# Performance work log

Hardware: AMD Instinct MI355X
Metric: run time of the kernel (lower is better)

Reference implementation:

```python
import jax, jax.numpy as jnp
import numpy as np

K = 10
ALPHA = 0.1
N_NODES = 100000
N_EDGES = 3200000
FEATURES = 512
HIDDEN = 256
CLASSES = 64


def setup_inputs() -> dict:
    key = jax.random.key(0)
    k1, k2, k3, k4 = jax.random.split(key, 4)
    x = jax.random.normal(k1, (N_NODES, FEATURES), dtype=jnp.float32)
    edge_index = jax.random.randint(k2, (2, N_EDGES), 0, N_NODES, dtype=jnp.int64)
    W1 = jax.random.normal(k3, (FEATURES, HIDDEN), dtype=jnp.float32) * (1.0 / np.sqrt(FEATURES))
    b1 = jnp.zeros((HIDDEN,), dtype=jnp.float32)
    W2 = jax.random.normal(k4, (HIDDEN, CLASSES), dtype=jnp.float32) * (1.0 / np.sqrt(HIDDEN))
    b2 = jnp.zeros((CLASSES,), dtype=jnp.float32)
    return {"x": x, "edge_index": edge_index, "W1": W1, "b1": b1, "W2": W2, "b2": b2}


def _gcn_norm(edge_index, n_nodes):
    # Add self-loops (APPNP / GCN normalization: D^-1/2 (A+I) D^-1/2)
    loops = jnp.arange(n_nodes, dtype=edge_index.dtype)
    row = jnp.concatenate([edge_index[0], loops])
    col = jnp.concatenate([edge_index[1], loops])
    ones = jnp.ones(row.shape[0], dtype=jnp.float32)
    deg = jax.ops.segment_sum(ones, col, num_segments=n_nodes)
    dinv = jnp.where(deg > 0, jax.lax.rsqrt(deg), 0.0)
    norm = dinv[row] * dinv[col]
    return row, col, norm


def reference(x, edge_index, W1, b1, W2, b2):
    n = x.shape[0]
    h = jax.nn.relu(x @ W1 + b1)          # [N, hidden]
    h = h @ W2 + b2                        # [N, classes]
    row, col, norm = _gcn_norm(edge_index, n)

    def step(out, _):
        msg = out[col] * norm[:, None]     # gather + scale over edges
        agg = jax.ops.segment_sum(msg, row, num_segments=n)
        return (1.0 - ALPHA) * agg + ALPHA * h, None

    out, _ = jax.lax.scan(step, h, None, length=K)
    return jax.nn.log_softmax(out, axis=1)
```

## Files before the change

### kernel.cpp

```cpp
#include <hip/hip_runtime.h>
#include <hip/hip_bf16.h>
#include <math.h>

#define N_NODES 100000
#define N_EDGES 3200000
#define FEAT 512
#define HID 256
#define CLS 64
#define K_ITER 10
#define NBUCK 196
#define BSH 9
#define CH 16384
#define NCHUNK 196

typedef _Float16 half8 __attribute__((ext_vector_type(8)));
typedef float f32x4 __attribute__((ext_vector_type(4)));

__device__ __forceinline__ int edge_at(const void* e, int is64, long long idx) {
    return is64 ? (int)((const long long*)e)[idx] : ((const int*)e)[idx];
}

__global__ void k_detect(const unsigned* __restrict__ e, int* __restrict__ flag,
                         int* __restrict__ bcntR, int* __restrict__ bcntC) {
    __shared__ unsigned s[256];
    unsigned v = 0;
    for (int i = threadIdx.x; i < 4096; i += 256) v |= e[2 * i + 1];
    s[threadIdx.x] = v;
    __syncthreads();
    for (int off = 128; off; off >>= 1) {
        if (threadIdx.x < off) s[threadIdx.x] |= s[threadIdx.x + off];
        __syncthreads();
    }
    if (threadIdx.x == 0) flag[0] = (s[0] == 0) ? 1 : 0;
    if (threadIdx.x < NBUCK) { bcntR[threadIdx.x] = 0; bcntC[threadIdx.x] = 0; }
}

__global__ __launch_bounds__(256) void k_bhist(const void* __restrict__ e,
                                               const int* __restrict__ flag,
                                               int* __restrict__ bcntR,
                                               int* __restrict__ bcntC,
                                               int* __restrict__ histR,
                                               int* __restrict__ histC) {
    __shared__ int lhR[NBUCK], lhC[NBUCK];
    for (int i = threadIdx.x; i < NBUCK; i += 256) { lhR[i] = 0; lhC[i] = 0; }
    __syncthreads();
    int is64 = flag[0];
    const int ch = blockIdx.x;
    long long base = (long long)ch * CH;
    for (int j = threadIdx.x; j < CH; j += 256) {
        long long i = base + j;
        if (i < N_EDGES) {
            int r = edge_at(e, is64, i);
            int c = edge_at(e, is64, (long long)N_EDGES + i);
            atomicAdd(&lhR[r >> BSH], 1);
            atomicAdd(&lhC[c >> BSH], 1);
        }
    }
    __syncthreads();
    for (int i = threadIdx.x; i < NBUCK; i += 256) {
        histR[ch * NBUCK + i] = lhR[i];
        histC[ch * NBUCK + i] = lhC[i];
        if (lhR[i]) atomicAdd(&bcntR[i], lhR[i]);
        if (lhC[i]) atomicAdd(&bcntC[i], lhC[i]);
    }
}

__global__ void k_bscan(const int* __restrict__ bcntR, const int* __restrict__ bcntC,
                        int* __restrict__ bbaseR, int* __restrict__ bbaseC,
                        int* __restrict__ cbase, int* __restrict__ offs) {
    if (threadIdx.x == 0) {
        int accE = 0, accC = 0, accCv = 0;
        for (int b = 0; b < NBUCK; b++) {
            bbaseR[b] = accE;
            bbaseC[b] = accCv;
            cbase[b] = accC;
            int nb0 = b << BSH;
            int nn = (N_NODES - nb0 < 512) ? (N_NODES - nb0) : 512;
            accE += bcntR[b];
            accCv += bcntC[b];
            accC += bcntR[b] + nn;
        }
        bbaseR[NBUCK] = accE;
        bbaseC[NBUCK] = accCv;
        cbase[NBUCK] = accC;
        offs[N_NODES] = accC;
    }
}

__global__ __launch_bounds__(256) void k_bscan2(const int* __restrict__ histR,
                                                const int* __restrict__ bbaseR,
                                                int* __restrict__ baseR,
                                                const int* __restrict__ histC,
                                                const int* __restrict__ bbaseC,
                                                int* __restrict__ baseC) {
    __shared__ int s[256];
    const int t = threadIdx.x;
    const int* hist;
    const int* bb;
    int* bout;
    int b;
    if (blockIdx.x < NBUCK) { hist = histR; bb = bbaseR; bout = baseR; b = blockIdx.x; }
    else { hist = histC; bb = bbaseC; bout = baseC; b = blockIdx.x - NBUCK; }
    int v = (t < NCHUNK) ? hist[t * NBUCK + b] : 0;
    s[t] = v;
    __syncthreads();
    for (int off = 1; off < 256; off <<= 1) {
        int a = (t >= off) ? s[t - off] : 0;
        __syncthreads();
        s[t] += a;
        __syncthreads();
    }
    if (t < NCHUNK) bout[t * NBUCK + b] = bb[b] + s[t] - v;
}

__global__ __launch_bounds__(256) void k_binA(const void* __restrict__ e,
                                              const int* __restrict__ flag,
                                              const int* __restrict__ baseR,
                                              const int* __restrict__ baseC,
                                              unsigned* __restrict__ pairs,
                                              int* __restrict__ cvals) {
    __shared__ int lbR[NBUCK], lcR[NBUCK], lbC[NBUCK], lcC[NBUCK];
    const int ch = blockIdx.x;
    for (int i = threadIdx.x; i < NBUCK; i += 256) {
        lbR[i] = baseR[ch * NBUCK + i];
        lcR[i] = 0;
        lbC[i] = baseC[ch * NBUCK + i];
        lcC[i] = 0;
    }
    __syncthreads();
    int is64 = flag[0];
    long long base = (long long)ch * CH;
    for (int j = threadIdx.x; j < CH; j += 256) {
        long long i = base + j;
        if (i < N_EDGES) {
            int r = edge_at(e, is64, i);
            int c = edge_at(e, is64, (long long)N_EDGES + i);
            int b = r >> BSH;
            int pos = atomicAdd(&lcR[b], 1);
            pairs[(long long)lbR[b] + pos] = ((unsigned)c << 9) | (unsigned)(r & 511);
            int bc = c >> BSH;
            int posc = atomicAdd(&lcC[bc], 1);
            cvals[(long long)lbC[bc] + posc] = c;
        }
    }
}

__global__ __launch_bounds__(1024) void k_bins(const int* __restrict__ cvals,
                                               const int* __restrict__ bbaseC,
                                               float* __restrict__ dinv,
                                               const unsigned* __restrict__ pairs,
                                               const int* __restrict__ bbaseR,
                                               const int* __restrict__ cbase,
                                               int* __restrict__ offs,
                                               int* __restrict__ ccol) {
    __shared__ int cnt[512], cur[512], s[512];
    const int t = threadIdx.x;
    if (blockIdx.x < NBUCK) {
        const int b = blockIdx.x;
        const int nb0 = b << BSH;
        const int nn = (N_NODES - nb0 < 512) ? (N_NODES - nb0) : 512;
        if (t < 512) cnt[t] = 1;
        __syncthreads();
        const int e0 = bbaseC[b], e1 = bbaseC[b + 1];
        for (int i = e0 + t; i < e1; i += 1024) {
            atomicAdd(&cnt[cvals[i] - nb0], 1);
        }
        __syncthreads();
        if (t < nn) dinv[nb0 + t] = rsqrtf((float)cnt[t]);
        return;
    }
    const int b = blockIdx.x - NBUCK;
    const int nb0 = b << BSH;
    const int nn = (N_NODES - nb0 < 512) ? (N_NODES - nb0) : 512;
    if (t < 512) cnt[t] = (t < nn) ? 1 : 0;
    __syncthreads();
    const int e0 = bbaseR[b], e1 = bbaseR[b + 1];
    for (int i = e0 + t; i < e1; i += 1024) {
        atomicAdd(&cnt[pairs[i] & 511u], 1);
    }
    __syncthreads();
    int v = (t < 512) ? cnt[t] : 0;
    if (t < 512) s[t] = v;
    __syncthreads();
    for (int off = 1; off < 512; off <<= 1) {
        int a = 0;
        if (t < 512 && t >= off) a = s[t - off];
        __syncthreads();
        if (t < 512) s[t] += a;
        __syncthreads();
    }
    const int cb = cbase[b];
    if (t < 512) {
        int excl = s[t] - v;
        cur[t] = excl;
        if (t < nn) {
            offs[nb0 + t] = cb + excl;
            ccol[cb + excl] = nb0 + t;
            cur[t] = excl + 1;
        }
    }
    __syncthreads();
    for (int i = e0 + t; i < e1; i += 1024) {
        unsigned p = pairs[i];
        int r = (int)(p & 511u);
        int c = (int)(p >> 9);
        int pos = atomicAdd(&cur[r], 1);
        ccol[cb + pos] = c;
    }
}

__global__ void k_cvtW(const float* __restrict__ W1, const float* __restrict__ W2,
                       _Float16* __restrict__ W1T, _Float16* __restrict__ W2T) {
    int i = blockIdx.x * 256 + threadIdx.x;
    if (i < 256 * 512) {
        int n = i >> 9, k = i & 511;
        W1T[i] = (_Float16)W1[k * 256 + n];
    }
    if (i < 64 * 256) {
        int n = i >> 8, k = i & 255;
        W2T[i] = (_Float16)W2[k * 64 + n];
    }
}

__device__ __forceinline__ int swz(int row, int g) {
    return g ^ (row & 3) ^ ((row >> 2) & 3);
}

__global__ __launch_bounds__(512) void k_gemm1(const float* __restrict__ A,
                                               const _Float16* __restrict__ BT,
                                               const float* __restrict__ bias,
                                               _Float16* __restrict__ C, int M) {
    __shared__ __align__(16) char lds[8192 + 16384];
    const int t = threadIdx.x;
    const int wid = t >> 6, lane = t & 63;
    const int wr = wid >> 2, wc = wid & 3;
    const int srow = t >> 2, sg = t & 3;
    const int fr = lane & 15, fg = lane >> 4;
    const long long by = blockIdx.x;

    f32x4 acc[4][4] = {};
    const long long arow = by * 128 + srow;
    const bool avalid = (arow < M);
    const float* ap0 = A + arow * FEAT + sg * 8;

    for (int kt = 0; kt < FEAT; kt += 32) {
        float4 a0 = make_float4(0.f, 0.f, 0.f, 0.f), a1 = a0;
        if (avalid) {
            const float* ap = ap0 + kt;
            a0 = *(const float4*)ap;
            a1 = *(const float4*)(ap + 4);
        }
        half8 ah;
        ah[0] = (_Float16)a0.x; ah[1] = (_Float16)a0.y;
        ah[2] = (_Float16)a0.z; ah[3] = (_Float16)a0.w;
        ah[4] = (_Float16)a1.x; ah[5] = (_Float16)a1.y;
        ah[6] = (_Float16)a1.z; ah[7] = (_Float16)a1.w;
        *(half8*)(lds + srow * 64 + swz(srow, sg) * 16) = ah;
#pragma unroll
        for (int rep = 0; rep < 2; rep++) {
            int brow = rep * 128 + srow;
            half8 bh = *(const half8*)(BT + brow * FEAT + kt + sg * 8);
            *(half8*)(lds + 8192 + brow * 64 + swz(brow, sg) * 16) = bh;
        }
        __syncthreads();

        half8 af[4], bf[4];
#pragma unroll
        for (int mi = 0; mi < 4; mi++) {
            int r = wr * 64 + mi * 16 + fr;
            af[mi] = *(const half8*)(lds + r * 64 + swz(r, fg) * 16);
        }
#pragma unroll
        for (int nj = 0; nj < 4; nj++) {
            int r = wc * 64 + nj * 16 + fr;
            bf[nj] = *(const half8*)(lds + 8192 + r * 64 + swz(r, fg) * 16);
        }
#pragma unroll
        for (int mi = 0; mi < 4; mi++)
#pragma unroll
            for (int nj = 0; nj < 4; nj++)
                acc[mi][nj] = __builtin_amdgcn_mfma_f32_16x16x32_f16(af[mi], bf[nj], acc[mi][nj], 0, 0, 0);
        __syncthreads();
    }

#pragma unroll
    for (int mi = 0; mi < 4; mi++) {
#pragma unroll
        for (int nj = 0; nj < 4; nj++) {
            int col = wc * 64 + nj * 16 + fr;
            float bv = bias[col];
#pragma unroll
            for (int r = 0; r < 4; r++) {
                long long row = by * 128 + wr * 64 + mi * 16 + fg * 4 + r;
                if (row < M) {
                    float v = fmaxf(acc[mi][nj][r] + bv, 0.f);
                    C[row * HID + col] = (_Float16)v;
                }
            }
        }
    }
}

__global__ __launch_bounds__(512) void k_gemm2(const _Float16* __restrict__ A,
                                               const _Float16* __restrict__ BT,
                                               const float* __restrict__ bias,
                                               const float* __restrict__ dinv,
                                               _Float16* __restrict__ Hout,
                                               _Float16* __restrict__ S0, int M) {
    __shared__ __align__(16) char lds[16384 + 4096];
    const int t = threadIdx.x;
    const int wid = t >> 6, lane = t & 63;
    const int wr = wid >> 1, wc = wid & 1;
    const int srow = t >> 2, sg = t & 3;
    const int fr = lane & 15, fg = lane >> 4;
    const long long bm = blockIdx.x;

    f32x4 acc[4][2] = {};

    for (int kt = 0; kt < HID; kt += 32) {
#pragma unroll
        for (int rep = 0; rep < 2; rep++) {
            int ar = rep * 128 + srow;
            long long grow = bm * 256 + ar;
            if (grow >= M) grow = M - 1;
            half8 ah = *(const half8*)(A + grow * HID + kt + sg * 8);
            *(half8*)(lds + ar * 64 + swz(ar, sg) * 16) = ah;
        }
        if (t < 256) {
            int br = t >> 2;
            half8 bh = *(const half8*)(BT + br * HID + kt + sg * 8);
            *(half8*)(lds + 16384 + br * 64 + swz(br, sg) * 16) = bh;
        }
        __syncthreads();

        half8 af[4], bf[2];
#pragma unroll
        for (int mi = 0; mi < 4; mi++) {
            int r = wr * 64 + mi * 16 + fr;
            af[mi] = *(const half8*)(lds + r * 64 + swz(r, fg) * 16);
        }
#pragma unroll
        for (int nj = 0; nj < 2; nj++) {
            int r = wc * 32 + nj * 16 + fr;
            bf[nj] = *(const half8*)(lds + 16384 + r * 64 + swz(r, fg) * 16);
        }
#pragma unroll
        for (int mi = 0; mi < 4; mi++)
#pragma unroll
            for (int nj = 0; nj < 2; nj++)
                acc[mi][nj] = __builtin_amdgcn_mfma_f32_16x16x32_f16(af[mi], bf[nj], acc[mi][nj], 0, 0, 0);
        __syncthreads();
    }

#pragma unroll
    for (int mi = 0; mi < 4; mi++) {
#pragma unroll
        for (int nj = 0; nj < 2; nj++) {
            int col = wc * 32 + nj * 16 + fr;
            float bv = bias[col];
#pragma unroll
            for (int r = 0; r < 4; r++) {
                long long row = bm * 256 + wr * 64 + mi * 16 + fg * 4 + r;
                if (row < M) {
                    float o = acc[mi][nj][r] + bv;
                    Hout[row * CLS + col] = (_Float16)o;
                    S0[row * CLS + col] = (_Float16)(dinv[row] * o);
                }
            }
        }
    }
}

__global__ __launch_bounds__(256) void k_prop(const int* __restrict__ ccol,
                                              const int* __restrict__ offs,
                                              const float* __restrict__ dinv,
                                              const _Float16* __restrict__ src,
                                              const _Float16* __restrict__ h,
                                              _Float16* __restrict__ dst,
                                              float* __restrict__ out, int last) {
    int wid = (blockIdx.x << 2) + (threadIdx.x >> 6);
    int lane = threadIdx.x & 63;
    if (wid >= N_NODES) return;
    const int g = lane >> 3;
    const int sl = lane & 7;
    const int e0 = offs[wid], e1 = offs[wid + 1];
    float acc[8] = {};
    int e = e0;
    for (; e + 32 <= e1; e += 32) {
        int c0 = ccol[e + g];
        int c1 = ccol[e + 8 + g];
        int c2 = ccol[e + 16 + g];
        int c3 = ccol[e + 24 + g];
        half8 v0 = *(const half8*)(src + (long long)c0 * CLS + sl * 8);
        half8 v1 = *(const half8*)(src + (long long)c1 * CLS + sl * 8);
        half8 v2 = *(const half8*)(src + (long long)c2 * CLS + sl * 8);
        half8 v3 = *(const half8*)(src + (long long)c3 * CLS + sl * 8);
#pragma unroll
        for (int j = 0; j < 8; j++)
            acc[j] += ((float)v0[j] + (float)v1[j]) + ((float)v2[j] + (float)v3[j]);
    }
    if (e + 16 <= e1) {
        int c0 = ccol[e + g];
        int c1 = ccol[e + 8 + g];
        half8 v0 = *(const half8*)(src + (long long)c0 * CLS + sl * 8);
        half8 v1 = *(const half8*)(src + (long long)c1 * CLS + sl * 8);
#pragma unroll
        for (int j = 0; j < 8; j++) acc[j] += (float)v0[j] + (float)v1[j];
        e += 16;
    }
    if (e + 8 <= e1) {
        int c0 = ccol[e + g];
        half8 v0 = *(const half8*)(src + (long long)c0 * CLS + sl * 8);
#pragma unroll
        for (int j = 0; j < 8; j++) acc[j] += (float)v0[j];
        e += 8;
    }
    if (e < e1) {
        int idx = e + g;
        if (idx < e1) {
            int c = ccol[idx];
            half8 v = *(const half8*)(src + (long long)c * CLS + sl * 8);
#pragma unroll
            for (int j = 0; j < 8; j++) acc[j] += (float)v[j];
        }
    }
#pragma unroll
    for (int j = 0; j < 8; j++) {
        acc[j] += __shfl_xor(acc[j], 8);
        acc[j] += __shfl_xor(acc[j], 16);
        acc[j] += __shfl_xor(acc[j], 32);
    }

    float dr = dinv[wid];
    half8 hh = *(const half8*)(h + (long long)wid * CLS + sl * 8);
    float o[8];
#pragma unroll
    for (int j = 0; j < 8; j++) o[j] = 0.9f * dr * acc[j] + 0.1f * (float)hh[j];

    if (!last) {
        if (g == 0) {
            half8 ov;
#pragma unroll
            for (int j = 0; j < 8; j++) ov[j] = (_Float16)(dr * o[j]);
            *(half8*)(dst + (long long)wid * CLS + sl * 8) = ov;
        }
    } else {
        float m = o[0];
#pragma unroll
        for (int j = 1; j < 8; j++) m = fmaxf(m, o[j]);
        m = fmaxf(m, __shfl_xor(m, 1));
        m = fmaxf(m, __shfl_xor(m, 2));
        m = fmaxf(m, __shfl_xor(m, 4));
        float s = 0.f;
#pragma unroll
        for (int j = 0; j < 8; j++) s += expf(o[j] - m);
        s += __shfl_xor(s, 1);
        s += __shfl_xor(s, 2);
        s += __shfl_xor(s, 4);
        float ls = logf(s);
        if (g == 0) {
            float4 ov0 = make_float4(o[0] - m - ls, o[1] - m - ls, o[2] - m - ls, o[3] - m - ls);
            float4 ov1 = make_float4(o[4] - m - ls, o[5] - m - ls, o[6] - m - ls, o[7] - m - ls);
            *(float4*)(out + (long long)wid * CLS + sl * 8) = ov0;
            *(float4*)(out + (long long)wid * CLS + sl * 8 + 4) = ov1;
        }
    }
}

extern "C" void kernel_launch(void* const* d_in, const int* in_sizes, int n_in,
                              void* d_out, int out_size, void* d_ws, size_t ws_size,
                              hipStream_t stream) {
    const float* x  = (const float*)d_in[0];
    const void*  ei = d_in[1];
    const float* W1 = (const float*)d_in[2];
    const float* b1 = (const float*)d_in[3];
    const float* W2 = (const float*)d_in[4];
    const float* b2 = (const float*)d_in[5];
    float* out = (float*)d_out;

    char* p = (char*)d_ws;
    size_t off = 0;
    auto alloc = [&](size_t bytes) {
        char* q = p + off;
        off = (off + bytes + 255) & ~(size_t)255;
        return q;
    };
    int*      flag   = (int*)alloc(16);
    float*    dinv   = (float*)alloc((size_t)N_NODES * 4);
    int*      offs   = (int*)alloc((size_t)(N_NODES + 1) * 4);
    int*      bcntR  = (int*)alloc((NBUCK + 1) * 4);
    int*      bcntC  = (int*)alloc((NBUCK + 1) * 4);
    int*      bbaseR = (int*)alloc((NBUCK + 1) * 4);
    int*      bbaseC = (int*)alloc((NBUCK + 1) * 4);
    int*      cbase  = (int*)alloc((NBUCK + 1) * 4);
    int*      histR  = (int*)alloc((size_t)NCHUNK * NBUCK * 4);
    int*      histC  = (int*)alloc((size_t)NCHUNK * NBUCK * 4);
    int*      baseR  = (int*)alloc((size_t)NCHUNK * NBUCK * 4);
    int*      baseC  = (int*)alloc((size_t)NCHUNK * NBUCK * 4);
    unsigned* pairs  = (unsigned*)alloc((size_t)N_EDGES * 4);
    int*      cvals  = (int*)alloc((size_t)N_EDGES * 4);
    int*      ccol   = (int*)alloc(((size_t)N_EDGES + N_NODES + 64) * 4);
    _Float16* h      = (_Float16*)alloc((size_t)N_NODES * CLS * 2);
    _Float16* s0     = (_Float16*)alloc((size_t)N_NODES * CLS * 2);
    _Float16* bufA   = (_Float16*)alloc((size_t)N_NODES * CLS * 2);
    _Float16* bufB   = (_Float16*)alloc((size_t)N_NODES * CLS * 2);
    _Float16* h1     = (_Float16*)alloc((size_t)N_NODES * HID * 2);
    _Float16* W1T    = (_Float16*)alloc((size_t)HID * FEAT * 2);
    _Float16* W2T    = (_Float16*)alloc((size_t)CLS * HID * 2);
    (void)ws_size;

    k_detect<<<1, 256, 0, stream>>>((const unsigned*)ei, flag, bcntR, bcntC);
    k_bhist<<<NCHUNK, 256, 0, stream>>>(ei, flag, bcntR, bcntC, histR, histC);
    k_bscan<<<1, 64, 0, stream>>>(bcntR, bcntC, bbaseR, bbaseC, cbase, offs);
    k_bscan2<<<2 * NBUCK, 256, 0, stream>>>(histR, bbaseR, baseR, histC, bbaseC, baseC);
    k_binA<<<NCHUNK, 256, 0, stream>>>(ei, flag, baseR, baseC, pairs, cvals);
    k_bins<<<2 * NBUCK, 1024, 0, stream>>>(cvals, bbaseC, dinv, pairs, bbaseR, cbase, offs, ccol);

    k_cvtW<<<512, 256, 0, stream>>>(W1, W2, W1T, W2T);
    k_gemm1<<<(N_NODES + 127) / 128, 512, 0, stream>>>(x, W1T, b1, h1, N_NODES);
    k_gemm2<<<(N_NODES + 255) / 256, 512, 0, stream>>>(h1, W2T, b2, dinv, h, s0, N_NODES);

    const int pgrid = (N_NODES + 3) / 4;
    _Float16* ping[2] = {bufA, bufB};
    for (int it = 0; it < K_ITER; it++) {
        const _Float16* src = (it == 0) ? s0 : ping[(it - 1) & 1];
        _Float16* dst = ping[it & 1];
        k_prop<<<pgrid, 256, 0, stream>>>(ccol, offs, dinv, src, h, dst, out, it == K_ITER - 1);
    }
}
```

Before: 772.8 us.

## Fuse ten propagation launches into one persistent cooperative kernel with grid sync

Replaces the ten per-iteration k_prop launches with a single cooperative persistent kernel. Waves grid-stride over nodes and call a grid-wide barrier between iterations, with the ping-pong buffers selected inside the kernel. The goal is to remove launch overhead and the tail drain of each kernel boundary. In exchange it adds grid-sync cost and limits the grid to resident occupancy, which can reduce latency hiding for the gathers, and it makes host occupancy and device-property queries on every call.

New measurement: 1.922 ms. 2.49x slower.

```diff
diff --git a/kernel.cpp b/kernel.cpp
--- a/kernel.cpp
+++ b/kernel.cpp
@@ -1,6 +1,9 @@
 #include <hip/hip_runtime.h>
 #include <hip/hip_bf16.h>
+#include <hip/hip_cooperative_groups.h>
 #include <math.h>
+
+namespace cg = cooperative_groups;
 
 #define N_NODES 100000
 #define N_EDGES 3200000
@@ -371,99 +374,111 @@
     }
 }
 
-__global__ __launch_bounds__(256) void k_prop(const int* __restrict__ ccol,
-                                              const int* __restrict__ offs,
-                                              const float* __restrict__ dinv,
-                                              const _Float16* __restrict__ src,
-                                              const _Float16* __restrict__ h,
-                                              _Float16* __restrict__ dst,
-                                              float* __restrict__ out, int last) {
-    int wid = (blockIdx.x << 2) + (threadIdx.x >> 6);
-    int lane = threadIdx.x & 63;
-    if (wid >= N_NODES) return;
+__global__ __launch_bounds__(256) void k_prop_all(const int* __restrict__ ccol,
+                                                  const int* __restrict__ offs,
+                                                  const float* __restrict__ dinv,
+                                                  const _Float16* __restrict__ s0,
+                                                  const _Float16* __restrict__ h,
+                                                  _Float16* __restrict__ bufA,
+                                                  _Float16* __restrict__ bufB,
+                                                  float* __restrict__ out,
+                                                  int nwaves) {
+    cg::grid_group gg = cg::this_grid();
+    const int gw = (blockIdx.x << 2) + (threadIdx.x >> 6);
+    const int lane = threadIdx.x & 63;
     const int g = lane >> 3;
     const int sl = lane & 7;
-    const int e0 = offs[wid], e1 = offs[wid + 1];
-    float acc[8] = {};
-    int e = e0;
-    for (; e + 32 <= e1; e += 32) {
-        int c0 = ccol[e + g];
-        int c1 = ccol[e + 8 + g];
-        int c2 = ccol[e + 16 + g];
-        int c3 = ccol[e + 24 + g];
-        half8 v0 = *(const half8*)(src + (long long)c0 * CLS + sl * 8);
-        half8 v1 = *(const half8*)(src + (long long)c1 * CLS + sl * 8);
-        half8 v2 = *(const half8*)(src + (long long)c2 * CLS + sl * 8);
-        half8 v3 = *(const half8*)(src + (long long)c3 * CLS + sl * 8);
-#pragma unroll
-        for (int j = 0; j < 8; j++)
-            acc[j] += ((float)v0[j] + (float)v1[j]) + ((float)v2[j] + (float)v3[j]);
-    }
-    if (e + 16 <= e1) {
-        int c0 = ccol[e + g];
-        int c1 = ccol[e + 8 + g];
-        half8 v0 = *(const half8*)(src + (long long)c0 * CLS + sl * 8);
-        half8 v1 = *(const half8*)(src + (long long)c1 * CLS + sl * 8);
-#pragma unroll
-        for (int j = 0; j < 8; j++) acc[j] += (float)v0[j] + (float)v1[j];
-        e += 16;
-    }
-    if (e + 8 <= e1) {
-        int c0 = ccol[e + g];
-        half8 v0 = *(const half8*)(src + (long long)c0 * CLS + sl * 8);
-#pragma unroll
-        for (int j = 0; j < 8; j++) acc[j] += (float)v0[j];
-        e += 8;
-    }
-    if (e < e1) {
-        int idx = e + g;
-        if (idx < e1) {
-            int c = ccol[idx];
-            half8 v = *(const half8*)(src + (long long)c * CLS + sl * 8);
-#pragma unroll
-            for (int j = 0; j < 8; j++) acc[j] += (float)v[j];
-        }
-    }
-#pragma unroll
-    for (int j = 0; j < 8; j++) {
-        acc[j] += __shfl_xor(acc[j], 8);
-        acc[j] += __shfl_xor(acc[j], 16);
-        acc[j] += __shfl_xor(acc[j], 32);
-    }
-
-    float dr = dinv[wid];
-    half8 hh = *(const half8*)(h + (long long)wid * CLS + sl * 8);
-    float o[8];
-#pragma unroll
-    for (int j = 0; j < 8; j++) o[j] = 0.9f * dr * acc[j] + 0.1f * (float)hh[j];
-
-    if (!last) {
-        if (g == 0) {
-            half8 ov;
-#pragma unroll
-            for (int j = 0; j < 8; j++) ov[j] = (_Float16)(dr * o[j]);
-            *(half8*)(dst + (long long)wid * CLS + sl * 8) = ov;
-        }
-    } else {
-        float m = o[0];
-#pragma unroll
-        for (int j = 1; j < 8; j++) m = fmaxf(m, o[j]);
-        m = fmaxf(m, __shfl_xor(m, 1));
-        m = fmaxf(m, __shfl_xor(m, 2));
-        m = fmaxf(m, __shfl_xor(m, 4));
-        float s = 0.f;
-#pragma unroll
-        for (int j = 0; j < 8; j++) s += expf(o[j] - m);
-        s += __shfl_xor(s, 1);
-        s += __shfl_xor(s, 2);
-        s += __shfl_xor(s, 4);
-        float ls = logf(s);
-        if (g == 0) {
-            float4 ov0 = make_float4(o[0] - m - ls, o[1] - m - ls, o[2] - m - ls, o[3] - m - ls);
-            float4 ov1 = make_float4(o[4] - m - ls, o[5] - m - ls, o[6] - m - ls, o[7] - m - ls);
-            *(float4*)(out + (long long)wid * CLS + sl * 8) = ov0;
-            *(float4*)(out + (long long)wid * CLS + sl * 8 + 4) = ov1;
-        }
+
+    for (int it = 0; it < K_ITER; it++) {
+        const _Float16* src = (it == 0) ? s0 : ((it & 1) ? bufA : bufB);
+        _Float16* dst = (it & 1) ? bufB : bufA;
+        const int last = (it == K_ITER - 1);
+
+        for (int wid = gw; wid < N_NODES; wid += nwaves) {
+            const int e0 = offs[wid], e1 = offs[wid + 1];
+            float acc[8] = {};
+            int e = e0;
+            for (; e + 32 <= e1; e += 32) {
+                int c0 = ccol[e + g];
+                int c1 = ccol[e + 8 + g];
+                int c2 = ccol[e + 16 + g];
+                int c3 = ccol[e + 24 + g];
+                half8 v0 = *(const half8*)(src + (long long)c0 * CLS + sl * 8);
+                half8 v1 = *(const half8*)(src + (long long)c1 * CLS + sl * 8);
+                half8 v2 = *(const half8*)(src + (long long)c2 * CLS + sl * 8);
+                half8 v3 = *(const half8*)(src + (long long)c3 * CLS + sl * 8);
+#pragma unroll
+                for (int j = 0; j < 8; j++)
+                    acc[j] += ((float)v0[j] + (float)v1[j]) + ((float)v2[j] + (float)v3[j]);
+            }
+            if (e + 16 <= e1) {
+                int c0 = ccol[e + g];
+                int c1 = ccol[e + 8 + g];
+                half8 v0 = *(const half8*)(src + (long long)c0 * CLS + sl * 8);
+                half8 v1 = *(const half8*)(src + (long long)c1 * CLS + sl * 8);
+#pragma unroll
+                for (int j = 0; j < 8; j++) acc[j] += (float)v0[j] + (float)v1[j];
+                e += 16;
+            }
+            if (e + 8 <= e1) {
+                int c0 = ccol[e + g];
+                half8 v0 = *(const half8*)(src + (long long)c0 * CLS + sl * 8);
+#pragma unroll
+                for (int j = 0; j < 8; j++) acc[j] += (float)v0[j];
+                e += 8;
+            }
+            if (e < e1) {
+                int idx = e + g;
+                if (idx < e1) {
+                    int c = ccol[idx];
+                    half8 v = *(const half8*)(src + (long long)c * CLS + sl * 8);
+#pragma unroll
+                    for (int j = 0; j < 8; j++) acc[j] += (float)v[j];
+                }
+            }
+#pragma unroll
+            for (int j = 0; j < 8; j++) {
+                acc[j] += __shfl_xor(acc[j], 8);
+                acc[j] += __shfl_xor(acc[j], 16);
+                acc[j] += __shfl_xor(acc[j], 32);
+            }
+
+            float dr = dinv[wid];
+            half8 hh = *(const half8*)(h + (long long)wid * CLS + sl * 8);
+            float o[8];
+#pragma unroll
+            for (int j = 0; j < 8; j++) o[j] = 0.9f * dr * acc[j] + 0.1f * (float)hh[j];
+
+            if (!last) {
+                if (g == 0) {
+                    half8 ov;
+#pragma unroll
+                    for (int j = 0; j < 8; j++) ov[j] = (_Float16)(dr * o[j]);
+                    *(half8*)(dst + (long long)wid * CLS + sl * 8) = ov;
+                }
+            } else {
+                float m = o[0];
+#pragma unroll
+                for (int j = 1; j < 8; j++) m = fmaxf(m, o[j]);
+                m = fmaxf(m, __shfl_xor(m, 1));
+                m = fmaxf(m, __shfl_xor(m, 2));
+                m = fmaxf(m, __shfl_xor(m, 4));
+                float s = 0.f;
+#pragma unroll
+                for (int j = 0; j < 8; j++) s += expf(o[j] - m);
+                s += __shfl_xor(s, 1);
+                s += __shfl_xor(s, 2);
+                s += __shfl_xor(s, 4);
+                float ls = logf(s);
+                if (g == 0) {
+                    float4 ov0 = make_float4(o[0] - m - ls, o[1] - m - ls, o[2] - m - ls, o[3] - m - ls);
+                    float4 ov1 = make_float4(o[4] - m - ls, o[5] - m - ls, o[6] - m - ls, o[7] - m - ls);
+                    *(float4*)(out + (long long)wid * CLS + sl * 8) = ov0;
+                    *(float4*)(out + (long long)wid * CLS + sl * 8 + 4) = ov1;
+                }
+            }
+        }
+        if (!last) gg.sync();
     }
 }
 
@@ -520,11 +535,20 @@
     k_gemm1<<<(N_NODES + 127) / 128, 512, 0, stream>>>(x, W1T, b1, h1, N_NODES);
     k_gemm2<<<(N_NODES + 255) / 256, 512, 0, stream>>>(h1, W2T, b2, dinv, h, s0, N_NODES);
 
-    const int pgrid = (N_NODES + 3) / 4;
-    _Float16* ping[2] = {bufA, bufB};
-    for (int it = 0; it < K_ITER; it++) {
-        const _Float16* src = (it == 0) ? s0 : ping[(it - 1) & 1];
-        _Float16* dst = ping[it & 1];
-        k_prop<<<pgrid, 256, 0, stream>>>(ccol, offs, dinv, src, h, dst, out, it == K_ITER - 1);
-    }
-}
+    int blocksPerCU = 0;
+    hipOccupancyMaxActiveBlocksPerMultiprocessor(&blocksPerCU, k_prop_all, 256, 0);
+    if (blocksPerCU < 1) blocksPerCU = 1;
+    hipDeviceProp_t props;
+    int dev = 0;
+    hipGetDevice(&dev);
+    hipGetDeviceProperties(&props, dev);
+    int gridBlocks = blocksPerCU * props.multiProcessorCount;
+    int maxUseful = (N_NODES + 3) / 4;
+    if (gridBlocks > maxUseful) gridBlocks = maxUseful;
+    int nwaves = gridBlocks * 4;
+    void* args[] = {(void*)&ccol, (void*)&offs, (void*)&dinv, (void*)&s0,
+                    (void*)&h, (void*)&bufA, (void*)&bufB, (void*)&out,
+                    (void*)&nwaves};
+    hipLaunchCooperativeKernel((const void*)k_prop_all, dim3(gridBlocks), dim3(256),
+                               args, 0, stream);
+}
```

## Partition each node's CSR neighbor list into four source-index slices

Applied to the files above, without the earlier changes.

Builds a per-node 4-way split of the adjacency list by source node range (slices of 25000 nodes) during CSR construction. It stores the slice boundaries in a new offs2 array, and the propagation kernel walks the four segments in order. The aim is gather locality: neighbor reads in the same phase hit a narrower region of the source feature buffer, which should improve L2/MALL hit rates. The cost is extra bookkeeping in binning, more loop-tail overhead per node, and the loss of the 32-edge unrolled inner loop (now at most 16 per step).

Result: slower. 1.013 ms (+31.1%).

```diff
diff --git a/kernel.cpp b/kernel.cpp
--- a/kernel.cpp
+++ b/kernel.cpp
@@ -12,6 +12,7 @@
 #define BSH 9
 #define CH 16384
 #define NCHUNK 196
+#define SLICE 25000
 
 typedef _Float16 half8 __attribute__((ext_vector_type(8)));
 typedef float f32x4 __attribute__((ext_vector_type(4)));
@@ -152,60 +153,78 @@
                                                const int* __restrict__ bbaseR,
                                                const int* __restrict__ cbase,
                                                int* __restrict__ offs,
+                                               int4* __restrict__ offs2,
                                                int* __restrict__ ccol) {
-    __shared__ int cnt[512], cur[512], s[512];
+    __shared__ int cnt4[2048], cur4[2048], s[512];
     const int t = threadIdx.x;
     if (blockIdx.x < NBUCK) {
         const int b = blockIdx.x;
         const int nb0 = b << BSH;
         const int nn = (N_NODES - nb0 < 512) ? (N_NODES - nb0) : 512;
-        if (t < 512) cnt[t] = 1;
+        if (t < 512) cnt4[t] = 1;
         __syncthreads();
         const int e0 = bbaseC[b], e1 = bbaseC[b + 1];
         for (int i = e0 + t; i < e1; i += 1024) {
-            atomicAdd(&cnt[cvals[i] - nb0], 1);
-        }
-        __syncthreads();
-        if (t < nn) dinv[nb0 + t] = rsqrtf((float)cnt[t]);
+            atomicAdd(&cnt4[cvals[i] - nb0], 1);
+        }
+        __syncthreads();
+        if (t < nn) dinv[nb0 + t] = rsqrtf((float)cnt4[t]);
         return;
     }
     const int b = blockIdx.x - NBUCK;
     const int nb0 = b << BSH;
     const int nn = (N_NODES - nb0 < 512) ? (N_NODES - nb0) : 512;
-    if (t < 512) cnt[t] = (t < nn) ? 1 : 0;
+    for (int i = t; i < 2048; i += 1024) cnt4[i] = 0;
+    __syncthreads();
+    if (t < nn) cnt4[t * 4 + (nb0 + t) / SLICE] = 1;
     __syncthreads();
     const int e0 = bbaseR[b], e1 = bbaseR[b + 1];
-    for (int i = e0 + t; i < e1; i += 1024) {
-        atomicAdd(&cnt[pairs[i] & 511u], 1);
-    }
-    __syncthreads();
-    int v = (t < 512) ? cnt[t] : 0;
-    if (t < 512) s[t] = v;
-    __syncthreads();
-    for (int off = 1; off < 512; off <<= 1) {
-        int a = 0;
-        if (t < 512 && t >= off) a = s[t - off];
-        __syncthreads();
-        if (t < 512) s[t] += a;
-        __syncthreads();
-    }
-    const int cb = cbase[b];
-    if (t < 512) {
-        int excl = s[t] - v;
-        cur[t] = excl;
-        if (t < nn) {
-            offs[nb0 + t] = cb + excl;
-            ccol[cb + excl] = nb0 + t;
-            cur[t] = excl + 1;
-        }
-    }
-    __syncthreads();
     for (int i = e0 + t; i < e1; i += 1024) {
         unsigned p = pairs[i];
         int r = (int)(p & 511u);
         int c = (int)(p >> 9);
-        int pos = atomicAdd(&cur[r], 1);
-        ccol[cb + pos] = c;
+        atomicAdd(&cnt4[r * 4 + c / SLICE], 1);
+    }
+    __syncthreads();
+    int tot = 0;
+    if (t < 512)
+        tot = cnt4[t * 4] + cnt4[t * 4 + 1] + cnt4[t * 4 + 2] + cnt4[t * 4 + 3];
+    if (t < 512) s[t] = tot;
+    __syncthreads();
+    for (int off = 1; off < 512; off <<= 1) {
+        int a = 0;
+        if (t < 512 && t >= off) a = s[t - off];
+        __syncthreads();
+        if (t < 512) s[t] += a;
+        __syncthreads();
+    }
+    const int cb = cbase[b];
+    if (t < 512) {
+        int a0 = cb + s[t] - tot;
+        int a1 = a0 + cnt4[t * 4 + 0];
+        int a2 = a1 + cnt4[t * 4 + 1];
+        int a3 = a2 + cnt4[t * 4 + 2];
+        cur4[t * 4 + 0] = a0;
+        cur4[t * 4 + 1] = a1;
+        cur4[t * 4 + 2] = a2;
+        cur4[t * 4 + 3] = a3;
+        if (t < nn) {
+            int node = nb0 + t;
+            offs[node] = a0;
+            offs2[node] = make_int4(a0, a1, a2, a3);
+            int sb = node / SLICE;
+            int pos = cur4[t * 4 + sb];
+            cur4[t * 4 + sb] = pos + 1;
+            ccol[pos] = node;
+        }
+    }
+    __syncthreads();
+    for (int i = e0 + t; i < e1; i += 1024) {
+        unsigned p = pairs[i];
+        int r = (int)(p & 511u);
+        int c = (int)(p >> 9);
+        int pos = atomicAdd(&cur4[r * 4 + c / SLICE], 1);
+        ccol[pos] = c;
     }
 }
 
@@ -373,6 +392,7 @@
 
 __global__ __launch_bounds__(256) void k_prop(const int* __restrict__ ccol,
                                               const int* __restrict__ offs,
+                                              const int4* __restrict__ offs2,
                                               const float* __restrict__ dinv,
                                               const _Float16* __restrict__ src,
                                               const _Float16* __restrict__ h,
@@ -383,45 +403,38 @@
     if (wid >= N_NODES) return;
     const int g = lane >> 3;
     const int sl = lane & 7;
-    const int e0 = offs[wid], e1 = offs[wid + 1];
+    const int4 o2 = offs2[wid];
+    const int eend = offs[wid + 1];
+    int segs[5];
+    segs[0] = o2.x; segs[1] = o2.y; segs[2] = o2.z; segs[3] = o2.w; segs[4] = eend;
     float acc[8] = {};
-    int e = e0;
-    for (; e + 32 <= e1; e += 32) {
-        int c0 = ccol[e + g];
-        int c1 = ccol[e + 8 + g];
-        int c2 = ccol[e + 16 + g];
-        int c3 = ccol[e + 24 + g];
-        half8 v0 = *(const half8*)(src + (long long)c0 * CLS + sl * 8);
-        half8 v1 = *(const half8*)(src + (long long)c1 * CLS + sl * 8);
-        half8 v2 = *(const half8*)(src + (long long)c2 * CLS + sl * 8);
-        half8 v3 = *(const half8*)(src + (long long)c3 * CLS + sl * 8);
-#pragma unroll
-        for (int j = 0; j < 8; j++)
-            acc[j] += ((float)v0[j] + (float)v1[j]) + ((float)v2[j] + (float)v3[j]);
-    }
-    if (e + 16 <= e1) {
-        int c0 = ccol[e + g];
-        int c1 = ccol[e + 8 + g];
-        half8 v0 = *(const half8*)(src + (long long)c0 * CLS + sl * 8);
-        half8 v1 = *(const half8*)(src + (long long)c1 * CLS + sl * 8);
-#pragma unroll
-        for (int j = 0; j < 8; j++) acc[j] += (float)v0[j] + (float)v1[j];
-        e += 16;
-    }
-    if (e + 8 <= e1) {
-        int c0 = ccol[e + g];
-        half8 v0 = *(const half8*)(src + (long long)c0 * CLS + sl * 8);
-#pragma unroll
-        for (int j = 0; j < 8; j++) acc[j] += (float)v0[j];
-        e += 8;
-    }
-    if (e < e1) {
-        int idx = e + g;
-        if (idx < e1) {
-            int c = ccol[idx];
-            half8 v = *(const half8*)(src + (long long)c * CLS + sl * 8);
-#pragma unroll
-            for (int j = 0; j < 8; j++) acc[j] += (float)v[j];
+#pragma unroll
+    for (int blk = 0; blk < 4; blk++) {
+        int e = segs[blk];
+        const int bnd = segs[blk + 1];
+        for (; e + 16 <= bnd; e += 16) {
+            int c0 = ccol[e + g];
+            int c1 = ccol[e + 8 + g];
+            half8 v0 = *(const half8*)(src + (long long)c0 * CLS + sl * 8);
+            half8 v1 = *(const half8*)(src + (long long)c1 * CLS + sl * 8);
+#pragma unroll
+            for (int j = 0; j < 8; j++) acc[j] += (float)v0[j] + (float)v1[j];
+        }
+        if (e + 8 <= bnd) {
+            int c0 = ccol[e + g];
+            half8 v0 = *(const half8*)(src + (long long)c0 * CLS + sl * 8);
+#pragma unroll
+            for (int j = 0; j < 8; j++) acc[j] += (float)v0[j];
+            e += 8;
+        }
+        if (e < bnd) {
+            int idx = e + g;
+            if (idx < bnd) {
+                int c = ccol[idx];
+                half8 v = *(const half8*)(src + (long long)c * CLS + sl * 8);
+#pragma unroll
+                for (int j = 0; j < 8; j++) acc[j] += (float)v[j];
+            }
         }
     }
 #pragma unroll
@@ -488,6 +501,7 @@
     int*      flag   = (int*)alloc(16);
     float*    dinv   = (float*)alloc((size_t)N_NODES * 4);
     int*      offs   = (int*)alloc((size_t)(N_NODES + 1) * 4);
+    int4*     offs2  = (int4*)alloc((size_t)N_NODES * 16);
     int*      bcntR  = (int*)alloc((NBUCK + 1) * 4);
     int*      bcntC  = (int*)alloc((NBUCK + 1) * 4);
     int*      bbaseR = (int*)alloc((NBUCK + 1) * 4);
@@ -514,7 +528,8 @@
     k_bscan<<<1, 64, 0, stream>>>(bcntR, bcntC, bbaseR, bbaseC, cbase, offs);
     k_bscan2<<<2 * NBUCK, 256, 0, stream>>>(histR, bbaseR, baseR, histC, bbaseC, baseC);
     k_binA<<<NCHUNK, 256, 0, stream>>>(ei, flag, baseR, baseC, pairs, cvals);
-    k_bins<<<2 * NBUCK, 1024, 0, stream>>>(cvals, bbaseC, dinv, pairs, bbaseR, cbase, offs, ccol);
+    k_bins<<<2 * NBUCK, 1024, 0, stream>>>(cvals, bbaseC, dinv, pairs, bbaseR, cbase,
+                                           offs, offs2, ccol);
 
     k_cvtW<<<512, 256, 0, stream>>>(W1, W2, W1T, W2T);
     k_gemm1<<<(N_NODES + 127) / 128, 512, 0, stream>>>(x, W1T, b1, h1, N_NODES);
@@ -525,6 +540,7 @@
     for (int it = 0; it < K_ITER; it++) {
         const _Float16* src = (it == 0) ? s0 : ping[(it - 1) & 1];
         _Float16* dst = ping[it & 1];
-        k_prop<<<pgrid, 256, 0, stream>>>(ccol, offs, dinv, src, h, dst, out, it == K_ITER - 1);
-    }
-}
+        k_prop<<<pgrid, 256, 0, stream>>>(ccol, offs, offs2, dinv, src, h, dst, out,
+                                          it == K_ITER - 1);
+    }
+}
```
